# Optimization experiments

Measured on AMD Instinct MI355X. Metric: run time of the kernel, lower is better.

Reference implementation:

```python
import jax, jax.numpy as jnp
import numpy as np
from jax import lax

B, FREQ, TIME = 64, 128, 400
HID, STEPS, NCLS = 256, 50, 2
EPS = 1e-5
SLOPE = 25.0  # fast_sigmoid surrogate slope

@jax.custom_vjp
def spike(x):
    return (x > 0).astype(x.dtype)

def _spike_fwd(x):
    return (x > 0).astype(x.dtype), x

def _spike_bwd(x, g):
    return (g / (SLOPE * jnp.abs(x) + 1.0) ** 2,)

spike.defvjp(_spike_fwd, _spike_bwd)

def layernorm(x, g, b):
    m = x.mean(-1, keepdims=True)
    v = ((x - m) ** 2).mean(-1, keepdims=True)
    return (x - m) * lax.rsqrt(v + EPS) * g + b

def bn_eval(x, g, b, m, v):
    # eval-mode BatchNorm2d with running stats, x: (B,C,H,W)
    sh = (1, -1, 1, 1)
    return (x - m.reshape(sh)) * lax.rsqrt(v.reshape(sh) + EPS) * g.reshape(sh) + b.reshape(sh)

def conv3x3(x, w, b):
    y = lax.conv_general_dilated(x, w, (1, 1), 'SAME',
                                 dimension_numbers=('NCHW', 'OIHW', 'NCHW'))
    return y + b.reshape(1, -1, 1, 1)

def maxpool2(x):
    return lax.reduce_window(x, -jnp.inf, lax.max, (1, 1, 2, 2), (1, 1, 2, 2), 'VALID')

def interp_linear(h, out_size):
    # F.interpolate(mode='linear', align_corners=False); h: (B,C,Tin)
    Tin = h.shape[-1]
    src = (jnp.arange(out_size, dtype=h.dtype) + 0.5) * (Tin / out_size) - 0.5
    src = jnp.clip(src, 0.0, Tin - 1)
    lo = jnp.floor(src).astype(jnp.int32)
    hi = jnp.minimum(lo + 1, Tin - 1)
    w = src - lo.astype(h.dtype)
    return h[..., lo] * (1.0 - w) + h[..., hi] * w

def lif(cur, mem, beta, thr):
    # snntorch Leaky, reset_mechanism='subtract': reset from previous mem (detached)
    b = jnp.clip(beta, 0.0, 1.0)
    reset = lax.stop_gradient((mem > thr).astype(mem.dtype))
    mem = b * mem + cur - reset * thr
    spk = spike(mem - thr)
    return spk, mem

def setup_inputs() -> dict:
    key = jax.random.key(0)
    ks = jax.random.split(key, 8)
    rn = lambda k, s, sc: jax.random.normal(k, s, jnp.float32) * sc
    f32 = lambda v: jnp.asarray(v, jnp.float32)
    return dict(
        x=rn(ks[0], (B, 1, FREQ, TIME), 1.0),
        c1w=rn(ks[1], (32, 1, 3, 3), 0.3), c1b=jnp.zeros((32,), jnp.float32),
        bn1g=jnp.ones((32,), jnp.float32), bn1b=jnp.zeros((32,), jnp.float32),
        bn1m=jnp.zeros((32,), jnp.float32), bn1v=jnp.ones((32,), jnp.float32),
        c2w=rn(ks[2], (64, 32, 3, 3), 0.06), c2b=jnp.zeros((64,), jnp.float32),
        bn2g=jnp.ones((64,), jnp.float32), bn2b=jnp.zeros((64,), jnp.float32),
        bn2m=jnp.zeros((64,), jnp.float32), bn2v=jnp.ones((64,), jnp.float32),
        pw=rn(ks[3], (64, HID), 0.125), pb=jnp.zeros((HID,), jnp.float32),
        plg=jnp.ones((HID,), jnp.float32), plb=jnp.zeros((HID,), jnp.float32),
        ing=jnp.ones((HID,), jnp.float32), inb=jnp.zeros((HID,), jnp.float32),
        fc1w=rn(ks[4], (HID, HID), 0.0625), fc1b=jnp.zeros((HID,), jnp.float32),
        fc2w=rn(ks[5], (HID, HID // 2), 0.0625), fc2b=jnp.zeros((HID // 2,), jnp.float32),
        fcow=rn(ks[6], (HID // 2, NCLS), 0.0884), fcob=jnp.zeros((NCLS,), jnp.float32),
        beta1=f32(0.8), thr1=f32(1.0),
        beta2=f32(0.8), thr2=f32(1.0),
        beta3=f32(0.8), thr3=f32(1.0),
    )

def reference(x, c1w, c1b, bn1g, bn1b, bn1m, bn1v, c2w, c2b, bn2g, bn2b, bn2m, bn2v,
              pw, pb, plg, plb, ing, inb, fc1w, fc1b, fc2w, fc2b, fcow, fcob,
              beta1, thr1, beta2, thr2, beta3, thr3):
    Bb = x.shape[0]
    # encoder
    h = maxpool2(jax.nn.relu(bn_eval(conv3x3(x, c1w, c1b), bn1g, bn1b, bn1m, bn1v)))
    h = maxpool2(jax.nn.relu(bn_eval(conv3x3(h, c2w, c2b), bn2g, bn2b, bn2m, bn2v)))
    h = h.mean(axis=2)                 # (B, 64, T/4) mean over freq
    h = h.transpose(0, 2, 1)           # (B, T/4, 64)
    h = layernorm(h @ pw + pb, plg, plb)   # channel_proj + LN -> (B, T/4, HID)
    h = h.transpose(0, 2, 1)           # (B, HID, T/4)
    h = interp_linear(h, STEPS)        # (B, HID, STEPS)
    cur = layernorm(h.transpose(0, 2, 1), ing, inb)  # (B, STEPS, HID)
    # fc1 hoisted out of the time loop (depends only on currents)
    cur1 = jnp.einsum('bth,hk->btk', cur, fc1w) + fc1b  # (B, STEPS, HID)

    def step(carry, c1):
        m1, m2, mo = carry
        s1, m1 = lif(c1, m1, beta1, thr1)
        s2, m2 = lif(s1 @ fc2w + fc2b, m2, beta2, thr2)
        _, mo = lif(s2 @ fcow + fcob, mo, beta3, thr3)
        return (m1, m2, mo), (s1, mo)

    init = (jnp.zeros((Bb, HID), x.dtype),
            jnp.zeros((Bb, HID // 2), x.dtype),
            jnp.zeros((Bb, NCLS), x.dtype))
    _, (spk_rec, mo_rec) = lax.scan(step, init, cur1.transpose(1, 0, 2))
    logits = mo_rec.sum(0)                      # (B, NCLS)
    spike_record = spk_rec.transpose(1, 0, 2)   # (B, STEPS, HID)
    return logits, spike_record
```

## Files before the change

kernel.cpp:

```cpp
#include <hip/hip_runtime.h>
#include <math.h>

#define P1H 66
#define P1W 208
#define P1PLANE (P1H * P1W)


__global__ __launch_bounds__(256) void k0_border(float* __restrict__ p1p) {
  int plane = blockIdx.x;
  float* base = p1p + (size_t)plane * P1PLANE;
  for (int i = threadIdx.x; i < 544; i += 256) {
    int r, c;
    if (i < 208)      { r = 0;            c = i; }
    else if (i < 416) { r = 65;           c = i - 208; }
    else if (i < 480) { r = i - 416 + 1;  c = 0; }
    else              { r = i - 480 + 1;  c = 201; }
    base[r * P1W + c] = 0.f;
  }
}

__global__ __launch_bounds__(256) void k1_conv1(
    const float* __restrict__ x,  const float* __restrict__ c1w,
    const float* __restrict__ c1b, const float* __restrict__ g1,
    const float* __restrict__ b1, const float* __restrict__ m1,
    const float* __restrict__ v1, float* __restrict__ p1p) {
  __shared__ float tile[18][67];
  __shared__ float scale[32], shift[32];
  int wx = blockIdx.x, hy = blockIdx.y, b = blockIdx.z;
  int tid = threadIdx.x;
  int gy0 = hy * 16 - 1, gx0 = wx * 64 - 1;
  const float* xb = x + (size_t)b * 128 * 400;
  for (int i = tid; i < 18 * 66; i += 256) {
    int r = i / 66, c = i - r * 66;
    int gr = gy0 + r, gc = gx0 + c;
    float v = 0.f;
    if (gr >= 0 && gr < 128 && gc >= 0 && gc < 400) v = xb[gr * 400 + gc];
    tile[r][c] = v;
  }
  if (tid < 32) {
    double s = (double)g1[tid] / sqrt((double)v1[tid] + 1e-5);
    scale[tid] = (float)s;
    shift[tid] = (float)(((double)c1b[tid] - (double)m1[tid]) * s + (double)b1[tid]);
  }
  __syncthreads();
  int tx = tid & 31, ty = tid >> 5;
  int pw = wx * 32 + tx;
  int ph = hy * 8 + ty;
  if (pw >= 200) return;
  float in[4][4];
#pragma unroll
  for (int r = 0; r < 4; ++r)
#pragma unroll
    for (int c = 0; c < 4; ++c) in[r][c] = tile[2 * ty + r][2 * tx + c];
  for (int ch = 0; ch < 32; ++ch) {
    float s00 = 0, s01 = 0, s10 = 0, s11 = 0;
#pragma unroll
    for (int ky = 0; ky < 3; ++ky)
#pragma unroll
      for (int kx = 0; kx < 3; ++kx) {
        float w = c1w[ch * 9 + ky * 3 + kx];
        s00 = fmaf(w, in[ky][kx],     s00);
        s01 = fmaf(w, in[ky][kx + 1], s01);
        s10 = fmaf(w, in[ky + 1][kx],     s10);
        s11 = fmaf(w, in[ky + 1][kx + 1], s11);
      }
    float sc = scale[ch], sh = shift[ch];
    float y00 = fmaxf(fmaf(sc, s00, sh), 0.f);
    float y01 = fmaxf(fmaf(sc, s01, sh), 0.f);
    float y10 = fmaxf(fmaf(sc, s10, sh), 0.f);
    float y11 = fmaxf(fmaf(sc, s11, sh), 0.f);
    float r = fmaxf(fmaxf(y00, y01), fmaxf(y10, y11));
    p1p[((size_t)(b * 32 + ch) * P1H + (ph + 1)) * P1W + (pw + 1)] = r;
  }
}

__global__ __launch_bounds__(256, 6) void k2_conv2(
    const float* __restrict__ p1p, const float* __restrict__ c2w,
    const float* __restrict__ c2b, const float* __restrict__ g2,
    const float* __restrict__ b2, const float* __restrict__ m2,
    const float* __restrict__ v2, float* __restrict__ p2) {
  int b = blockIdx.z;
  int wid = __builtin_amdgcn_readfirstlane((int)(threadIdx.x >> 6));
  int lane = threadIdx.x & 63;
  int widx = blockIdx.x * 4 + wid;
  int ty = widx / 25, tx = widx - ty * 25;
  int r0 = ty * 4, c0 = tx * 8;
  const float* ipbase = p1p + (size_t)(b * 32) * P1PLANE + r0 * P1W + c0;
  float acc[4][8];
#pragma unroll
  for (int i = 0; i < 4; ++i)
#pragma unroll
    for (int j = 0; j < 8; ++j) acc[i][j] = 0.f;

  for (int ic = 0; ic < 32; ++ic) {
    float wv[9];
    const float* wp = c2w + ((lane * 32) + ic) * 9;
#pragma unroll
    for (int j = 0; j < 9; ++j) wv[j] = wp[j];
    const float* ip = ipbase + (size_t)ic * P1PLANE;
#pragma unroll
    for (int l = 0; l < 6; ++l) {
      float srow[10];
#pragma unroll
      for (int c = 0; c < 10; ++c) srow[c] = ip[l * P1W + c];
#pragma unroll
      for (int o = 0; o < 4; ++o) {
        int ky = l - o;
        if (ky >= 0 && ky <= 2) {
#pragma unroll
          for (int xo = 0; xo < 8; ++xo) {
            acc[o][xo] = fmaf(srow[xo + 0], wv[ky * 3 + 0], acc[o][xo]);
            acc[o][xo] = fmaf(srow[xo + 1], wv[ky * 3 + 1], acc[o][xo]);
            acc[o][xo] = fmaf(srow[xo + 2], wv[ky * 3 + 2], acc[o][xo]);
          }
        }
      }
    }
  }
  int oc = lane;
  double sd = (double)g2[oc] / sqrt((double)v2[oc] + 1e-5);
  float sc = (float)sd;
  float sh = (float)(((double)c2b[oc] - (double)m2[oc]) * sd + (double)b2[oc]);
#pragma unroll
  for (int py = 0; py < 2; ++py)
#pragma unroll
    for (int px = 0; px < 4; ++px) {
      float q00 = fmaxf(fmaf(sc, acc[2 * py][2 * px],         sh), 0.f);
      float q01 = fmaxf(fmaf(sc, acc[2 * py][2 * px + 1],     sh), 0.f);
      float q10 = fmaxf(fmaf(sc, acc[2 * py + 1][2 * px],     sh), 0.f);
      float q11 = fmaxf(fmaf(sc, acc[2 * py + 1][2 * px + 1], sh), 0.f);
      float r = fmaxf(fmaxf(q00, q01), fmaxf(q10, q11));
      p2[((size_t)(b * 64 + oc) * 32 + (ty * 2 + py)) * 100 + (tx * 4 + px)] = r;
    }
}

__global__ __launch_bounds__(256) void k3_mean(const float* __restrict__ p2,
                                               double* __restrict__ hm) {
  int idx = blockIdx.x * 256 + threadIdx.x;
  int xcol = idx % 100;
  int bc = idx / 100;
  const float* p = p2 + (size_t)bc * 3200 + xcol;
  double s = 0.0;
#pragma unroll
  for (int h = 0; h < 32; ++h) s += (double)p[h * 100];
  hm[idx] = s * (1.0 / 32.0);
}

__device__ __forceinline__ double block_reduce_sum_256(double v, double* sbuf) {
#pragma unroll
  for (int off = 32; off > 0; off >>= 1) v += __shfl_down(v, off, 64);
  int lane = threadIdx.x & 63, wid = threadIdx.x >> 6;
  __syncthreads();
  if (lane == 0) sbuf[wid] = v;
  __syncthreads();
  return sbuf[0] + sbuf[1] + sbuf[2] + sbuf[3];
}

__global__ __launch_bounds__(256) void k4_proj_ln(
    const double* __restrict__ hm, const float* __restrict__ pw,
    const float* __restrict__ pb, const float* __restrict__ plg,
    const float* __restrict__ plb, double* __restrict__ hproj) {
  __shared__ double sbuf[4];
  int bt0 = blockIdx.x * 4;
  int b = bt0 / 100, t0 = bt0 - b * 100;
  int k = threadIdx.x;
  double accv[4];
  double pbk = (double)pb[k];
#pragma unroll
  for (int r = 0; r < 4; ++r) accv[r] = pbk;
  const double* hmb = hm + (size_t)b * 64 * 100 + t0;
#pragma unroll 4
  for (int c = 0; c < 64; ++c) {
    double w = (double)pw[c * 256 + k];
    const double* hp = hmb + c * 100;
    accv[0] = fma(hp[0], w, accv[0]);
    accv[1] = fma(hp[1], w, accv[1]);
    accv[2] = fma(hp[2], w, accv[2]);
    accv[3] = fma(hp[3], w, accv[3]);
  }
  double gk = (double)plg[k], bk = (double)plb[k];
#pragma unroll
  for (int r = 0; r < 4; ++r) {
    double mean = block_reduce_sum_256(accv[r], sbuf) * (1.0 / 256.0);
    double d = accv[r] - mean;
    double var = block_reduce_sum_256(d * d, sbuf) * (1.0 / 256.0);
    double inv = 1.0 / sqrt(var + 1e-5);
    hproj[(size_t)(bt0 + r) * 256 + k] = d * inv * gk + bk;
  }
}

__global__ __launch_bounds__(256) void k5a_interp_ln(
    const double* __restrict__ hproj, const float* __restrict__ ing,
    const float* __restrict__ inb, double* __restrict__ curs) {
  __shared__ double sbuf[4];
  int bs = blockIdx.x;
  int b = bs / 50, st = bs - b * 50;
  int k = threadIdx.x;
  const double* hp = hproj + (size_t)(b * 100 + 2 * st) * 256;
  double xk = 0.5 * (hp[k] + hp[256 + k]);
  double mean = block_reduce_sum_256(xk, sbuf) * (1.0 / 256.0);
  double d = xk - mean;
  double var = block_reduce_sum_256(d * d, sbuf) * (1.0 / 256.0);
  double inv = 1.0 / sqrt(var + 1e-5);
  curs[(size_t)bs * 256 + k] = d * inv * (double)ing[k] + (double)inb[k];
}

__global__ __launch_bounds__(256) void k5b_fc1(
    const double* __restrict__ curs, const float* __restrict__ fc1w,
    const float* __restrict__ fc1b, double* __restrict__ cur1) {
  int row0 = blockIdx.x * 8;
  int k = threadIdx.x;
  double accv[8];
  double bk = (double)fc1b[k];
#pragma unroll
  for (int r = 0; r < 8; ++r) accv[r] = bk;
  const double* ab = curs + (size_t)row0 * 256;
#pragma unroll 4
  for (int c = 0; c < 256; ++c) {
    double w = (double)fc1w[c * 256 + k];
#pragma unroll
    for (int r = 0; r < 8; ++r)
      accv[r] = fma(ab[(size_t)r * 256 + c], w, accv[r]);
  }
#pragma unroll
  for (int r = 0; r < 8; ++r) cur1[(size_t)(row0 + r) * 256 + k] = accv[r];
}

__global__ __launch_bounds__(64) void k6_lif1(
    const double* __restrict__ cur1, const float* __restrict__ beta1p,
    const float* __restrict__ thr1p, float* __restrict__ dout) {
  int b = blockIdx.x >> 2;
  int k = ((blockIdx.x & 3) << 6) + threadIdx.x;
  double beta = (double)beta1p[0];
  beta = beta < 0.0 ? 0.0 : (beta > 1.0 ? 1.0 : beta);
  double thr = (double)thr1p[0];
  double mem = 0.0;
  float* srec = dout + 128;
  for (int t = 0; t < 50; ++t) {
    double c = cur1[(size_t)(b * 50 + t) * 256 + k];
    mem = beta * mem + c - ((mem > thr) ? thr : 0.0);
    srec[(size_t)(b * 50 + t) * 256 + k] = (mem > thr) ? 1.0f : 0.0f;
  }
}

__global__ __launch_bounds__(128) void k7_fc2(
    const float* __restrict__ dout, const float* __restrict__ fc2w,
    const float* __restrict__ fc2b, double* __restrict__ cur2) {
  int row0 = blockIdx.x * 8;
  int j = threadIdx.x;
  const float* srec = dout + 128;
  double accv[8];
  double bj = (double)fc2b[j];
#pragma unroll
  for (int r = 0; r < 8; ++r) accv[r] = bj;
#pragma unroll 4
  for (int c = 0; c < 256; ++c) {
    double w = (double)fc2w[c * 128 + j];
#pragma unroll
    for (int r = 0; r < 8; ++r)
      accv[r] = fma((double)srec[(size_t)(row0 + r) * 256 + c], w, accv[r]);
  }
#pragma unroll
  for (int r = 0; r < 8; ++r) cur2[(size_t)(row0 + r) * 128 + j] = accv[r];
}

__global__ __launch_bounds__(64) void k8a_lif2(
    const double* __restrict__ cur2, const float* __restrict__ beta2p,
    const float* __restrict__ thr2p, float* __restrict__ s2f) {
  int idx = blockIdx.x * 64 + threadIdx.x;
  int b = idx >> 7, j = idx & 127;
  double beta2 = (double)beta2p[0];
  beta2 = beta2 < 0.0 ? 0.0 : (beta2 > 1.0 ? 1.0 : beta2);
  double thr2 = (double)thr2p[0];
  double m2 = 0.0;
  for (int t = 0; t < 50; ++t) {
    double c2 = cur2[(size_t)(b * 50 + t) * 128 + j];
    m2 = beta2 * m2 + c2 - ((m2 > thr2) ? thr2 : 0.0);
    s2f[(size_t)(b * 50 + t) * 128 + j] = (m2 > thr2) ? 1.0f : 0.0f;
  }
}

__global__ __launch_bounds__(64) void k8b_out(
    const float* __restrict__ s2f, const float* __restrict__ fcow,
    const float* __restrict__ fcob, const float* __restrict__ beta3p,
    const float* __restrict__ thr3p, float* __restrict__ dout) {
  __shared__ double c3s[50][2];
  int b = blockIdx.x, t = threadIdx.x;
  if (t < 50) {
    double c30 = (double)fcob[0], c31 = (double)fcob[1];
    const float* sp = s2f + (size_t)(b * 50 + t) * 128;
#pragma unroll 4
    for (int jj = 0; jj < 128; ++jj) {
      double s = (double)sp[jj];
      c30 = fma(s, (double)fcow[jj * 2 + 0], c30);
      c31 = fma(s, (double)fcow[jj * 2 + 1], c31);
    }
    c3s[t][0] = c30; c3s[t][1] = c31;
  }
  __syncthreads();
  if (t == 0) {
    double beta3 = (double)beta3p[0];
    beta3 = beta3 < 0.0 ? 0.0 : (beta3 > 1.0 ? 1.0 : beta3);
    double thr3 = (double)thr3p[0];
    double mo0 = 0.0, mo1 = 0.0, l0 = 0.0, l1 = 0.0;
    for (int tt = 0; tt < 50; ++tt) {
      mo0 = beta3 * mo0 + c3s[tt][0] - ((mo0 > thr3) ? thr3 : 0.0);
      mo1 = beta3 * mo1 + c3s[tt][1] - ((mo1 > thr3) ? thr3 : 0.0);
      l0 += mo0; l1 += mo1;
    }
    dout[b * 2 + 0] = (float)l0; dout[b * 2 + 1] = (float)l1;
  }
}

extern "C" void kernel_launch(void* const* d_in, const int* in_sizes, int n_in,
                              void* d_out, int out_size, void* d_ws, size_t ws_size,
                              hipStream_t stream) {
  const float* x    = (const float*)d_in[0];
  const float* c1w  = (const float*)d_in[1];
  const float* c1b  = (const float*)d_in[2];
  const float* bn1g = (const float*)d_in[3];
  const float* bn1b = (const float*)d_in[4];
  const float* bn1m = (const float*)d_in[5];
  const float* bn1v = (const float*)d_in[6];
  const float* c2w  = (const float*)d_in[7];
  const float* c2b  = (const float*)d_in[8];
  const float* bn2g = (const float*)d_in[9];
  const float* bn2b = (const float*)d_in[10];
  const float* bn2m = (const float*)d_in[11];
  const float* bn2v = (const float*)d_in[12];
  const float* pw   = (const float*)d_in[13];
  const float* pb   = (const float*)d_in[14];
  const float* plg  = (const float*)d_in[15];
  const float* plb  = (const float*)d_in[16];
  const float* ing  = (const float*)d_in[17];
  const float* inb  = (const float*)d_in[18];
  const float* fc1w = (const float*)d_in[19];
  const float* fc1b = (const float*)d_in[20];
  const float* fc2w = (const float*)d_in[21];
  const float* fc2b = (const float*)d_in[22];
  const float* fcow = (const float*)d_in[23];
  const float* fcob = (const float*)d_in[24];
  const float* beta1 = (const float*)d_in[25];
  const float* thr1  = (const float*)d_in[26];
  const float* beta2 = (const float*)d_in[27];
  const float* thr2  = (const float*)d_in[28];
  const float* beta3 = (const float*)d_in[29];
  const float* thr3  = (const float*)d_in[30];

  char* ws = (char*)d_ws;
  float*  p1p   = (float*)ws;
  float*  p2    = (float*)(ws + 112459776ULL);
  double* hm    = (double*)ws;
  double* hproj = (double*)(ws + 3276800ULL);
  double* curs  = (double*)(ws + 16384000ULL);
  double* cur1  = (double*)(ws + 22937600ULL);
  double* cur2  = (double*)(ws + 29491200ULL);
  float*  s2f   = (float*)(ws + 32768000ULL);
  float* dout = (float*)d_out;

  k0_border<<<dim3(2048), 256, 0, stream>>>(p1p);
  k1_conv1<<<dim3(7, 8, 64), 256, 0, stream>>>(x, c1w, c1b, bn1g, bn1b, bn1m, bn1v, p1p);
  k2_conv2<<<dim3(100, 1, 64), 256, 0, stream>>>(p1p, c2w, c2b, bn2g, bn2b, bn2m, bn2v, p2);
  k3_mean<<<dim3(1600), 256, 0, stream>>>(p2, hm);
  k4_proj_ln<<<dim3(1600), 256, 0, stream>>>(hm, pw, pb, plg, plb, hproj);
  k5a_interp_ln<<<dim3(3200), 256, 0, stream>>>(hproj, ing, inb, curs);
  k5b_fc1<<<dim3(400), 256, 0, stream>>>(curs, fc1w, fc1b, cur1);
  k6_lif1<<<dim3(256), 64, 0, stream>>>(cur1, beta1, thr1, dout);
  k7_fc2<<<dim3(400), 128, 0, stream>>>(dout, fc2w, fc2b, cur2);
  k8a_lif2<<<dim3(128), 64, 0, stream>>>(cur2, beta2, thr2, s2f);
  k8b_out<<<dim3(64), 64, 0, stream>>>(s2f, fcow, fcob, beta3, thr3, dout);
}
```

Before: 584.7 us.

## Remap conv2 to pixel-per-lane with transposed weights and fuse mean and tail kernels

Conv2 now gives each lane one output pixel and loops over output channels in two passes of 32. It reads pre-transposed weights that are uniform across the wave, computes BN/ReLU and the 2x2 maxpool through lane shuffles, and runs with a higher occupancy bound. A new prep kernel transposes the conv2 weights and precomputes the BN2 scale and shift, and the padded plane width shrinks from 208 to 204. The freq-mean is fused into the projection+LN kernel through shared memory, and the LIF2 and output-layer kernels are merged into one per-batch kernel that keeps spikes in LDS. These changes remove launches and global round-trips and aim to improve conv2 weight reuse, at the cost of redundant loads of the input neighbourhood and more register pressure.

```diff
diff --git a/kernel.cpp b/kernel.cpp
--- a/kernel.cpp
+++ b/kernel.cpp
@@ -2,19 +2,38 @@
 #include <math.h>
 
 #define P1H 66
-#define P1W 208
+#define P1W 204
 #define P1PLANE (P1H * P1W)
 
+
+__global__ __launch_bounds__(256) void kw_prep(
+    const float* __restrict__ c2w, const float* __restrict__ c2b,
+    const float* __restrict__ g2, const float* __restrict__ b2,
+    const float* __restrict__ m2, const float* __restrict__ v2,
+    float* __restrict__ c2wT, float* __restrict__ bn2sc, float* __restrict__ bn2sh) {
+  int blk = blockIdx.x;
+  if (blk < 72) {
+    int d = blk * 256 + threadIdx.x;
+    int ic = d / 576, rem = d - ic * 576;
+    int oc = rem / 9, t = rem - oc * 9;
+    c2wT[d] = c2w[(oc * 32 + ic) * 9 + t];
+  } else if (threadIdx.x < 64) {
+    int o = threadIdx.x;
+    double sd = (double)g2[o] / sqrt((double)v2[o] + 1e-5);
+    bn2sc[o] = (float)sd;
+    bn2sh[o] = (float)(((double)c2b[o] - (double)m2[o]) * sd + (double)b2[o]);
+  }
+}
 
 __global__ __launch_bounds__(256) void k0_border(float* __restrict__ p1p) {
   int plane = blockIdx.x;
   float* base = p1p + (size_t)plane * P1PLANE;
-  for (int i = threadIdx.x; i < 544; i += 256) {
+  for (int i = threadIdx.x; i < 536; i += 256) {
     int r, c;
-    if (i < 208)      { r = 0;            c = i; }
-    else if (i < 416) { r = 65;           c = i - 208; }
-    else if (i < 480) { r = i - 416 + 1;  c = 0; }
-    else              { r = i - 480 + 1;  c = 201; }
+    if (i < 204)      { r = 0;            c = i; }
+    else if (i < 408) { r = 65;           c = i - 204; }
+    else if (i < 472) { r = i - 408 + 1;  c = 0; }
+    else              { r = i - 472 + 1;  c = 201; }
     base[r * P1W + c] = 0.f;
   }
 }
@@ -74,119 +93,118 @@
   }
 }
 
-__global__ __launch_bounds__(256, 6) void k2_conv2(
-    const float* __restrict__ p1p, const float* __restrict__ c2w,
-    const float* __restrict__ c2b, const float* __restrict__ g2,
-    const float* __restrict__ b2, const float* __restrict__ m2,
-    const float* __restrict__ v2, float* __restrict__ p2) {
+__global__ __launch_bounds__(256, 8) void k2_conv2(
+    const float* __restrict__ p1p, const float* __restrict__ c2wT,
+    const float* __restrict__ bn2sc, const float* __restrict__ bn2sh,
+    float* __restrict__ p2) {
   int b = blockIdx.z;
-  int wid = __builtin_amdgcn_readfirstlane((int)(threadIdx.x >> 6));
+  int tile = blockIdx.x;
+  int rt = tile / 13, ct = tile - rt * 13;
+  int wave = threadIdx.x >> 6;
   int lane = threadIdx.x & 63;
-  int widx = blockIdx.x * 4 + wid;
-  int ty = widx / 25, tx = widx - ty * 25;
-  int r0 = ty * 4, c0 = tx * 8;
-  const float* ipbase = p1p + (size_t)(b * 32) * P1PLANE + r0 * P1W + c0;
-  float acc[4][8];
-#pragma unroll
-  for (int i = 0; i < 4; ++i)
-#pragma unroll
-    for (int j = 0; j < 8; ++j) acc[i][j] = 0.f;
-
-  for (int ic = 0; ic < 32; ++ic) {
-    float wv[9];
-    const float* wp = c2w + ((lane * 32) + ic) * 9;
-#pragma unroll
-    for (int j = 0; j < 9; ++j) wv[j] = wp[j];
-    const float* ip = ipbase + (size_t)ic * P1PLANE;
-#pragma unroll
-    for (int l = 0; l < 6; ++l) {
-      float srow[10];
-#pragma unroll
-      for (int c = 0; c < 10; ++c) srow[c] = ip[l * P1W + c];
-#pragma unroll
-      for (int o = 0; o < 4; ++o) {
-        int ky = l - o;
-        if (ky >= 0 && ky <= 2) {
-#pragma unroll
-          for (int xo = 0; xo < 8; ++xo) {
-            acc[o][xo] = fmaf(srow[xo + 0], wv[ky * 3 + 0], acc[o][xo]);
-            acc[o][xo] = fmaf(srow[xo + 1], wv[ky * 3 + 1], acc[o][xo]);
-            acc[o][xo] = fmaf(srow[xo + 2], wv[ky * 3 + 2], acc[o][xo]);
-          }
-        }
+  int rl = lane >> 4, cl = lane & 15;
+  int r = rt * 16 + wave * 4 + rl;
+  int c = ct * 16 + cl;
+  const float* pb0 = p1p + (size_t)(b * 32) * P1PLANE;
+  int voff = r * P1W + c;
+
+#pragma unroll
+  for (int pass = 0; pass < 2; ++pass) {
+    int ocb = pass * 32;
+    float acc[32];
+#pragma unroll
+    for (int o = 0; o < 32; ++o) acc[o] = 0.f;
+    for (int ic = 0; ic < 32; ++ic) {
+      const float* ip = pb0 + (size_t)ic * P1PLANE + voff;
+      float in[9];
+      in[0] = ip[0];            in[1] = ip[1];            in[2] = ip[2];
+      in[3] = ip[P1W];          in[4] = ip[P1W + 1];      in[5] = ip[P1W + 2];
+      in[6] = ip[2 * P1W];      in[7] = ip[2 * P1W + 1];  in[8] = ip[2 * P1W + 2];
+      const float* wp = c2wT + ((ic * 64) + ocb) * 9;
+#pragma unroll
+      for (int o = 0; o < 32; ++o) {
+#pragma unroll
+        for (int t = 0; t < 9; ++t)
+          acc[o] = fmaf(in[t], wp[o * 9 + t], acc[o]);
       }
     }
-  }
-  int oc = lane;
-  double sd = (double)g2[oc] / sqrt((double)v2[oc] + 1e-5);
-  float sc = (float)sd;
-  float sh = (float)(((double)c2b[oc] - (double)m2[oc]) * sd + (double)b2[oc]);
-#pragma unroll
-  for (int py = 0; py < 2; ++py)
-#pragma unroll
-    for (int px = 0; px < 4; ++px) {
-      float q00 = fmaxf(fmaf(sc, acc[2 * py][2 * px],         sh), 0.f);
-      float q01 = fmaxf(fmaf(sc, acc[2 * py][2 * px + 1],     sh), 0.f);
-      float q10 = fmaxf(fmaf(sc, acc[2 * py + 1][2 * px],     sh), 0.f);
-      float q11 = fmaxf(fmaf(sc, acc[2 * py + 1][2 * px + 1], sh), 0.f);
-      float r = fmaxf(fmaxf(q00, q01), fmaxf(q10, q11));
-      p2[((size_t)(b * 64 + oc) * 32 + (ty * 2 + py)) * 100 + (tx * 4 + px)] = r;
+    bool leader = ((lane & 1) == 0) && ((lane & 16) == 0);
+    int pr = r >> 1, pc = c >> 1;
+    bool valid = leader && (pc < 100);
+#pragma unroll
+    for (int o = 0; o < 32; ++o) {
+      int oc = ocb + o;
+      float y = fmaxf(bn2sc[oc] * acc[o] + bn2sh[oc], 0.f);
+      float a = fmaxf(y, __shfl_xor(y, 1, 64));
+      float m = fmaxf(a, __shfl_xor(a, 16, 64));
+      if (valid)
+        p2[((size_t)(b * 64 + oc) * 32 + pr) * 100 + pc] = m;
     }
-}
-
-__global__ __launch_bounds__(256) void k3_mean(const float* __restrict__ p2,
-                                               double* __restrict__ hm) {
-  int idx = blockIdx.x * 256 + threadIdx.x;
-  int xcol = idx % 100;
-  int bc = idx / 100;
-  const float* p = p2 + (size_t)bc * 3200 + xcol;
-  double s = 0.0;
-#pragma unroll
-  for (int h = 0; h < 32; ++h) s += (double)p[h * 100];
-  hm[idx] = s * (1.0 / 32.0);
-}
-
-__device__ __forceinline__ double block_reduce_sum_256(double v, double* sbuf) {
-#pragma unroll
-  for (int off = 32; off > 0; off >>= 1) v += __shfl_down(v, off, 64);
-  int lane = threadIdx.x & 63, wid = threadIdx.x >> 6;
-  __syncthreads();
-  if (lane == 0) sbuf[wid] = v;
-  __syncthreads();
-  return sbuf[0] + sbuf[1] + sbuf[2] + sbuf[3];
-}
-
-__global__ __launch_bounds__(256) void k4_proj_ln(
-    const double* __restrict__ hm, const float* __restrict__ pw,
+  }
+}
+
+__global__ __launch_bounds__(256) void k4_meanproj_ln(
+    const float* __restrict__ p2, const float* __restrict__ pw,
     const float* __restrict__ pb, const float* __restrict__ plg,
     const float* __restrict__ plb, double* __restrict__ hproj) {
+  __shared__ double hmld[64][4];
   __shared__ double sbuf[4];
   int bt0 = blockIdx.x * 4;
   int b = bt0 / 100, t0 = bt0 - b * 100;
-  int k = threadIdx.x;
+  int tid = threadIdx.x;
+  {
+    int cc = tid >> 2, rr = tid & 3;
+    const float* pp = p2 + (size_t)(b * 64 + cc) * 3200 + t0 + rr;
+    double s = 0.0;
+#pragma unroll
+    for (int h = 0; h < 32; ++h) s += (double)pp[h * 100];
+    hmld[cc][rr] = s * (1.0 / 32.0);
+  }
+  __syncthreads();
+  int k = tid;
   double accv[4];
   double pbk = (double)pb[k];
 #pragma unroll
   for (int r = 0; r < 4; ++r) accv[r] = pbk;
-  const double* hmb = hm + (size_t)b * 64 * 100 + t0;
 #pragma unroll 4
-  for (int c = 0; c < 64; ++c) {
-    double w = (double)pw[c * 256 + k];
-    const double* hp = hmb + c * 100;
-    accv[0] = fma(hp[0], w, accv[0]);
-    accv[1] = fma(hp[1], w, accv[1]);
-    accv[2] = fma(hp[2], w, accv[2]);
-    accv[3] = fma(hp[3], w, accv[3]);
+  for (int cc = 0; cc < 64; ++cc) {
+    double w = (double)pw[cc * 256 + k];
+    accv[0] = fma(hmld[cc][0], w, accv[0]);
+    accv[1] = fma(hmld[cc][1], w, accv[1]);
+    accv[2] = fma(hmld[cc][2], w, accv[2]);
+    accv[3] = fma(hmld[cc][3], w, accv[3]);
   }
   double gk = (double)plg[k], bk = (double)plb[k];
 #pragma unroll
   for (int r = 0; r < 4; ++r) {
-    double mean = block_reduce_sum_256(accv[r], sbuf) * (1.0 / 256.0);
+    double v = accv[r];
+#pragma unroll
+    for (int off = 32; off > 0; off >>= 1) v += __shfl_down(v, off, 64);
+    __syncthreads();
+    if ((tid & 63) == 0) sbuf[tid >> 6] = v;
+    __syncthreads();
+    double mean = (sbuf[0] + sbuf[1] + sbuf[2] + sbuf[3]) * (1.0 / 256.0);
     double d = accv[r] - mean;
-    double var = block_reduce_sum_256(d * d, sbuf) * (1.0 / 256.0);
+    double vv = d * d;
+#pragma unroll
+    for (int off = 32; off > 0; off >>= 1) vv += __shfl_down(vv, off, 64);
+    __syncthreads();
+    if ((tid & 63) == 0) sbuf[tid >> 6] = vv;
+    __syncthreads();
+    double var = (sbuf[0] + sbuf[1] + sbuf[2] + sbuf[3]) * (1.0 / 256.0);
     double inv = 1.0 / sqrt(var + 1e-5);
     hproj[(size_t)(bt0 + r) * 256 + k] = d * inv * gk + bk;
   }
+}
+
+__device__ __forceinline__ double block_reduce_sum_256(double v, double* sbuf) {
+#pragma unroll
+  for (int off = 32; off > 0; off >>= 1) v += __shfl_down(v, off, 64);
+  int lane = threadIdx.x & 63, wid = threadIdx.x >> 6;
+  __syncthreads();
+  if (lane == 0) sbuf[wid] = v;
+  __syncthreads();
+  return sbuf[0] + sbuf[1] + sbuf[2] + sbuf[3];
 }
 
 __global__ __launch_bounds__(256) void k5a_interp_ln(
@@ -264,11 +282,14 @@
   for (int r = 0; r < 8; ++r) cur2[(size_t)(row0 + r) * 128 + j] = accv[r];
 }
 
-__global__ __launch_bounds__(64) void k8a_lif2(
-    const double* __restrict__ cur2, const float* __restrict__ beta2p,
-    const float* __restrict__ thr2p, float* __restrict__ s2f) {
-  int idx = blockIdx.x * 64 + threadIdx.x;
-  int b = idx >> 7, j = idx & 127;
+__global__ __launch_bounds__(128) void k8_tail(
+    const double* __restrict__ cur2, const float* __restrict__ fcow,
+    const float* __restrict__ fcob, const float* __restrict__ beta2p,
+    const float* __restrict__ thr2p, const float* __restrict__ beta3p,
+    const float* __restrict__ thr3p, float* __restrict__ dout) {
+  __shared__ float s2s[50][128];
+  __shared__ double c3s[50][2];
+  int b = blockIdx.x, j = threadIdx.x;
   double beta2 = (double)beta2p[0];
   beta2 = beta2 < 0.0 ? 0.0 : (beta2 > 1.0 ? 1.0 : beta2);
   double thr2 = (double)thr2p[0];
@@ -276,29 +297,22 @@
   for (int t = 0; t < 50; ++t) {
     double c2 = cur2[(size_t)(b * 50 + t) * 128 + j];
     m2 = beta2 * m2 + c2 - ((m2 > thr2) ? thr2 : 0.0);
-    s2f[(size_t)(b * 50 + t) * 128 + j] = (m2 > thr2) ? 1.0f : 0.0f;
-  }
-}
-
-__global__ __launch_bounds__(64) void k8b_out(
-    const float* __restrict__ s2f, const float* __restrict__ fcow,
-    const float* __restrict__ fcob, const float* __restrict__ beta3p,
-    const float* __restrict__ thr3p, float* __restrict__ dout) {
-  __shared__ double c3s[50][2];
-  int b = blockIdx.x, t = threadIdx.x;
+    s2s[t][j] = (m2 > thr2) ? 1.0f : 0.0f;
+  }
+  __syncthreads();
+  int t = j;
   if (t < 50) {
     double c30 = (double)fcob[0], c31 = (double)fcob[1];
-    const float* sp = s2f + (size_t)(b * 50 + t) * 128;
 #pragma unroll 4
     for (int jj = 0; jj < 128; ++jj) {
-      double s = (double)sp[jj];
+      double s = (double)s2s[t][jj];
       c30 = fma(s, (double)fcow[jj * 2 + 0], c30);
       c31 = fma(s, (double)fcow[jj * 2 + 1], c31);
     }
     c3s[t][0] = c30; c3s[t][1] = c31;
   }
   __syncthreads();
-  if (t == 0) {
+  if (j == 0) {
     double beta3 = (double)beta3p[0];
     beta3 = beta3 < 0.0 ? 0.0 : (beta3 > 1.0 ? 1.0 : beta3);
     double thr3 = (double)thr3p[0];
@@ -349,24 +363,24 @@
 
   char* ws = (char*)d_ws;
   float*  p1p   = (float*)ws;
+  float*  c2wT  = (float*)(ws + 110297088ULL);
+  float*  bn2sc = (float*)(ws + 110370816ULL);
+  float*  bn2sh = (float*)(ws + 110371072ULL);
   float*  p2    = (float*)(ws + 112459776ULL);
-  double* hm    = (double*)ws;
   double* hproj = (double*)(ws + 3276800ULL);
   double* curs  = (double*)(ws + 16384000ULL);
   double* cur1  = (double*)(ws + 22937600ULL);
   double* cur2  = (double*)(ws + 29491200ULL);
-  float*  s2f   = (float*)(ws + 32768000ULL);
   float* dout = (float*)d_out;
 
+  kw_prep<<<dim3(73), 256, 0, stream>>>(c2w, c2b, bn2g, bn2b, bn2m, bn2v, c2wT, bn2sc, bn2sh);
   k0_border<<<dim3(2048), 256, 0, stream>>>(p1p);
   k1_conv1<<<dim3(7, 8, 64), 256, 0, stream>>>(x, c1w, c1b, bn1g, bn1b, bn1m, bn1v, p1p);
-  k2_conv2<<<dim3(100, 1, 64), 256, 0, stream>>>(p1p, c2w, c2b, bn2g, bn2b, bn2m, bn2v, p2);
-  k3_mean<<<dim3(1600), 256, 0, stream>>>(p2, hm);
-  k4_proj_ln<<<dim3(1600), 256, 0, stream>>>(hm, pw, pb, plg, plb, hproj);
+  k2_conv2<<<dim3(52, 1, 64), 256, 0, stream>>>(p1p, c2wT, bn2sc, bn2sh, p2);
+  k4_meanproj_ln<<<dim3(1600), 256, 0, stream>>>(p2, pw, pb, plg, plb, hproj);
   k5a_interp_ln<<<dim3(3200), 256, 0, stream>>>(hproj, ing, inb, curs);
   k5b_fc1<<<dim3(400), 256, 0, stream>>>(curs, fc1w, fc1b, cur1);
   k6_lif1<<<dim3(256), 64, 0, stream>>>(cur1, beta1, thr1, dout);
   k7_fc2<<<dim3(400), 128, 0, stream>>>(dout, fc2w, fc2b, cur2);
-  k8a_lif2<<<dim3(128), 64, 0, stream>>>(cur2, beta2, thr2, s2f);
-  k8b_out<<<dim3(64), 64, 0, stream>>>(s2f, fcow, fcob, beta3, thr3, dout);
-}
+  k8_tail<<<dim3(64), 128, 0, stream>>>(cur2, fcow, fcob, beta2, thr2, beta3, thr3, dout);
+}
```

New measurement: 787.1 us. +34.6%, slower.
